# Performance work log

Hardware: AMD Instinct MI355X
Metric: run time of the kernel (lower is better)

## Reference

```python
import jax, jax.numpy as jnp
import numpy as np

D_MODEL = 1024
EXPAND = 2
D_INNER = EXPAND * D_MODEL   # 2048
D_STATE = 16
D_CONV = 4
DT_RANK = 64                  # ceil(d_model / 16)
BATCH = 2
SEQLEN = 1024
DT_MIN, DT_MAX = 0.001, 0.1


def setup_inputs() -> dict:
    key = jax.random.key(0)
    ks = jax.random.split(key, 10)
    s = 0.02
    # dt bias init per Mamba: inv-softplus of dt sampled log-uniform in [dt_min, dt_max]
    u = jax.random.uniform(ks[0], (D_INNER,), jnp.float32)
    dt = jnp.exp(u * (np.log(DT_MAX) - np.log(DT_MIN)) + np.log(DT_MIN))
    dt = jnp.clip(dt, 1e-4, None)
    inv_dt = dt + jnp.log(-jnp.expm1(-dt))
    dt_std = DT_RANK ** -0.5
    A_log = jnp.log(jnp.tile(jnp.arange(1, D_STATE + 1, dtype=jnp.float32), (D_INNER, 1)))
    return {
        "hidden_states": jax.random.normal(ks[1], (BATCH, SEQLEN, D_MODEL), jnp.float32),
        "in_proj_w": jax.random.normal(ks[2], (2 * D_INNER, D_MODEL), jnp.float32) * s,
        "conv1d_w": jax.random.normal(ks[3], (D_INNER, D_CONV), jnp.float32) * s,
        "conv1d_b": jnp.zeros((D_INNER,), jnp.float32),
        "x_proj_w": jax.random.normal(ks[4], (DT_RANK + 2 * D_STATE, D_INNER), jnp.float32) * s,
        "dt_proj_w": jax.random.uniform(ks[5], (D_INNER, DT_RANK), jnp.float32, -dt_std, dt_std),
        "dt_proj_b": inv_dt,
        "A_log": A_log,
        "D_skip": jnp.ones((D_INNER,), jnp.float32),
        "out_proj_w": jax.random.normal(ks[6], (D_MODEL, D_INNER), jnp.float32) * s,
    }


def _mamba_forward(hidden_states, in_proj_w, conv1d_w, conv1d_b, x_proj_w,
                   dt_proj_w, dt_proj_b, A_log, D_skip, out_proj_w):
    B_, L, _ = hidden_states.shape
    # in_proj: (b, l, d_model) -> (b, l, 2*d_inner); split into x and gate z
    xz = jnp.einsum('bld,ed->ble', hidden_states, in_proj_w)
    x, z = xz[..., :D_INNER], xz[..., D_INNER:]
    # causal depthwise conv1d over time (pad left K-1, truncate to L) + SiLU
    xp = jnp.pad(x, ((0, 0), (D_CONV - 1, 0), (0, 0)))
    xc = conv1d_b
    acc = jnp.zeros_like(x)
    for k in range(D_CONV):  # tiny fixed kernel loop
        acc = acc + conv1d_w[:, k] * xp[:, k:k + L, :]
    xc = jax.nn.silu(acc + conv1d_b)
    # input-dependent dt / B / C
    x_dbl = jnp.einsum('bld,rd->blr', xc, x_proj_w)
    dt_lr = x_dbl[..., :DT_RANK]
    Bm = x_dbl[..., DT_RANK:DT_RANK + D_STATE]        # (b, l, n)
    Cm = x_dbl[..., DT_RANK + D_STATE:]               # (b, l, n)
    delta = jax.nn.softplus(jnp.einsum('blr,dr->bld', dt_lr, dt_proj_w) + dt_proj_b)
    A = -jnp.exp(A_log)                               # (d, n)

    def step(state, inputs):
        delta_t, B_t, C_t, u_t = inputs               # (b,d) (b,n) (b,n) (b,d)
        dA = jnp.exp(delta_t[..., None] * A)          # (b, d, n)
        state = state * dA + (delta_t * u_t)[..., None] * B_t[:, None, :]
        y_t = jnp.einsum('bdn,bn->bd', state, C_t)
        return state, y_t

    init = jnp.zeros((B_, D_INNER, D_STATE), delta.dtype)
    scan_in = (jnp.swapaxes(delta, 0, 1), jnp.swapaxes(Bm, 0, 1),
               jnp.swapaxes(Cm, 0, 1), jnp.swapaxes(xc, 0, 1))
    _, ys = jax.lax.scan(step, init, scan_in)         # ys: (l, b, d)
    y = jnp.swapaxes(ys, 0, 1)
    y = y + xc * D_skip                               # skip connection
    y = y * jax.nn.silu(z)                            # gate
    return jnp.einsum('bld,md->blm', y, out_proj_w)   # out_proj (no bias)


def reference(hidden_states, in_proj_w, conv1d_w, conv1d_b, x_proj_w,
              dt_proj_w, dt_proj_b, A_log, D_skip, out_proj_w):
    return _mamba_forward(hidden_states, in_proj_w, conv1d_w, conv1d_b, x_proj_w,
                          dt_proj_w, dt_proj_b, A_log, D_skip, out_proj_w)
```

## Files before the change

kernel.cpp:

```cpp
#include <hip/hip_runtime.h>
#include <hip/hip_bf16.h>
#include <math.h>
#include <stdint.h>

#define D_MODEL 1024
#define D_INNER 2048
#define D_STATE 16
#define D_CONV  4
#define DT_RANK 64
#define BATCH   2
#define SEQLEN  1024
#define M_TOK   (BATCH * SEQLEN)
#define XDBL_W  (DT_RANK + 2 * D_STATE)
#define CHUNKS  64
#define CLEN    (SEQLEN / CHUNKS)
#define KSPLIT  16
#define OSPLIT  4

typedef unsigned short us16;
typedef __bf16 bf16x8 __attribute__((ext_vector_type(8)));
typedef float floatx4 __attribute__((ext_vector_type(4)));

__device__ __forceinline__ float silu_f(float v) {
    return v / (1.0f + __expf(-v));
}
__device__ __forceinline__ float softplus_f(float v) {
    return v > 20.0f ? v : log1pf(__expf(v));
}
__device__ __forceinline__ us16 f2bf(float f) {
    unsigned u = __float_as_uint(f);
    u += 0x7FFF + ((u >> 16) & 1);
    return (us16)(u >> 16);
}
__device__ __forceinline__ float bf2f(us16 h) {
    return __uint_as_float(((unsigned)h) << 16);
}

__device__ __forceinline__ void gload_lds16(const us16* g, us16* l) {
    auto* l3 = reinterpret_cast<__attribute__((address_space(3))) us16*>(
        reinterpret_cast<uintptr_t>(l));
    auto* g1 = reinterpret_cast<const __attribute__((address_space(1))) us16*>(
        reinterpret_cast<uintptr_t>(g));
    __builtin_amdgcn_global_load_lds(g1, l3, 16, 0, 0);
}

__global__ __launch_bounds__(256)
void split_all(const float* __restrict__ hs, const float* __restrict__ iw,
               const float* __restrict__ ow,
               us16* __restrict__ hsh, us16* __restrict__ hsl,
               us16* __restrict__ iwh, us16* __restrict__ iwl,
               us16* __restrict__ owh, us16* __restrict__ owl)
{
    const int b = blockIdx.x;
    const float* src;
    us16 *hi, *lo;
    int rel;
    if (b < 2048)      { src = hs; hi = hsh; lo = hsl; rel = b; }
    else if (b < 6144) { src = iw; hi = iwh; lo = iwl; rel = b - 2048; }
    else               { src = ow; hi = owh; lo = owl; rel = b - 6144; }
    const int i = (rel * 256 + threadIdx.x) * 4;
    const float4 v = *(const float4*)(src + i);
    us16 h0 = f2bf(v.x), h1 = f2bf(v.y), h2 = f2bf(v.z), h3 = f2bf(v.w);
    ushort4 hv = {h0, h1, h2, h3};
    ushort4 lv = {f2bf(v.x - bf2f(h0)), f2bf(v.y - bf2f(h1)),
                  f2bf(v.z - bf2f(h2)), f2bf(v.w - bf2f(h3))};
    *(ushort4*)(hi + i) = hv;
    *(ushort4*)(lo + i) = lv;
}

template<int BN, int MODE>
__global__ __launch_bounds__(256)
void gemm_mfma3(const us16* __restrict__ Ah, const us16* __restrict__ Al,
                const us16* __restrict__ Wh, const us16* __restrict__ Wl,
                int lda, int kLen, float* __restrict__ C0,
                float* __restrict__ C1, int ldc)
{
    constexpr int BM = 128;
    constexpr int NT = BN / 32;
    __shared__ us16 sAh[BM * 32];
    __shared__ us16 sAl[BM * 32];
    __shared__ us16 sWh[BN * 32];
    __shared__ us16 sWl[BN * 32];

    const int tid  = threadIdx.x;
    const int wave = tid >> 6;
    const int lane = tid & 63;
    const int wm   = wave & 1;
    const int wn   = wave >> 1;
    const int m0   = blockIdx.y * BM;
    const int n0   = blockIdx.x * BN;
    const int kBeg = blockIdx.z * kLen;
    const int quad = lane >> 4;
    const int l15  = lane & 15;
    const int sr   = lane >> 2;
    const int spos = lane & 3;

    floatx4 acc[4][NT] = {};

    for (int k0 = 0; k0 < kLen; k0 += 32) {
        __syncthreads();
        {
            int s = wave;
            int row = s * 16 + sr;
            int c = spos ^ ((row >> 1) & 3);
            size_t go = (size_t)(m0 + row) * lda + kBeg + k0 + c * 8;
            gload_lds16(Ah + go, sAh + s * 512);
            gload_lds16(Al + go, sAl + s * 512);
            s = wave + 4;
            row = s * 16 + sr;
            c = spos ^ ((row >> 1) & 3);
            go = (size_t)(m0 + row) * lda + kBeg + k0 + c * 8;
            gload_lds16(Ah + go, sAh + s * 512);
            gload_lds16(Al + go, sAl + s * 512);
        }
        {
            int s = wave;
            int row = s * 16 + sr;
            int c = spos ^ ((row >> 1) & 3);
            size_t go = (size_t)(n0 + row) * lda + kBeg + k0 + c * 8;
            gload_lds16(Wh + go, sWh + s * 512);
            gload_lds16(Wl + go, sWl + s * 512);
            if (BN == 128) {
                s = wave + 4;
                row = s * 16 + sr;
                c = spos ^ ((row >> 1) & 3);
                go = (size_t)(n0 + row) * lda + kBeg + k0 + c * 8;
                gload_lds16(Wh + go, sWh + s * 512);
                gload_lds16(Wl + go, sWl + s * 512);
            }
        }
        __syncthreads();

        bf16x8 ah[4], al[4], bh[NT], bl[NT];
#pragma unroll
        for (int i = 0; i < 4; i++) {
            const int r = wm * 64 + i * 16 + l15;
            const int off = r * 32 + ((quad ^ ((r >> 1) & 3)) * 8);
            ah[i] = *(const bf16x8*)(sAh + off);
            al[i] = *(const bf16x8*)(sAl + off);
        }
#pragma unroll
        for (int j = 0; j < NT; j++) {
            const int r = wn * (BN / 2) + j * 16 + l15;
            const int off = r * 32 + ((quad ^ ((r >> 1) & 3)) * 8);
            bh[j] = *(const bf16x8*)(sWh + off);
            bl[j] = *(const bf16x8*)(sWl + off);
        }
#pragma unroll
        for (int i = 0; i < 4; i++)
#pragma unroll
            for (int j = 0; j < NT; j++) {
                acc[i][j] = __builtin_amdgcn_mfma_f32_16x16x32_bf16(
                    ah[i], bh[j], acc[i][j], 0, 0, 0);
                acc[i][j] = __builtin_amdgcn_mfma_f32_16x16x32_bf16(
                    al[i], bh[j], acc[i][j], 0, 0, 0);
                acc[i][j] = __builtin_amdgcn_mfma_f32_16x16x32_bf16(
                    ah[i], bl[j], acc[i][j], 0, 0, 0);
            }
    }

#pragma unroll
    for (int i = 0; i < 4; i++) {
        const int rowb = m0 + wm * 64 + i * 16 + quad * 4;
#pragma unroll
        for (int j = 0; j < NT; j++) {
            const int col = n0 + wn * (BN / 2) + j * 16 + l15;
#pragma unroll
            for (int r = 0; r < 4; r++) {
                const float v = acc[i][j][r];
                const size_t rr = (size_t)(rowb + r);
                if (MODE == 1) {
                    if (n0 < D_INNER) C0[rr * D_INNER + col] = v;
                    else              C1[rr * D_INNER + (col - D_INNER)] = v;
                } else {
                    C0[((size_t)blockIdx.z * M_TOK + rr) * ldc + col] = v;
                }
            }
        }
    }
}

__global__ __launch_bounds__(256)
void add4_kernel(const float* __restrict__ part, float* __restrict__ out)
{
    const int i = (blockIdx.x * 256 + threadIdx.x) * 4;
    const size_t stride = (size_t)M_TOK * D_MODEL;
    float4 a = *(const float4*)(part + i);
#pragma unroll
    for (int k = 1; k < OSPLIT; k++) {
        const float4 b = *(const float4*)(part + k * stride + i);
        a.x += b.x; a.y += b.y; a.z += b.z; a.w += b.w;
    }
    *(float4*)(out + i) = a;
}

__global__ __launch_bounds__(256)
void gemm_dt(const float* __restrict__ A, int lda,
             const float* __restrict__ W, int ldw,
             float* __restrict__ C0, int ldc,
             const float* __restrict__ bias, int K)
{
    __shared__ float As[16][68];
    __shared__ float Ws[16][68];

    const int tid  = threadIdx.x;
    const int tx   = tid & 15;
    const int ty   = tid >> 4;
    const int n0   = blockIdx.x * 64;
    const int m0   = blockIdx.y * 64;
    const int lrow = tid >> 2;
    const int lkq  = tid & 3;

    float acc[4][4] = {};

    for (int k0 = 0; k0 < K; k0 += 16) {
        const float4 av = *(const float4*)(A + (size_t)(m0 + lrow) * lda + k0 + lkq * 4);
        const float4 wv = *(const float4*)(W + (size_t)(n0 + lrow) * ldw + k0 + lkq * 4);

        __syncthreads();
        As[lkq * 4 + 0][lrow] = av.x;
        As[lkq * 4 + 1][lrow] = av.y;
        As[lkq * 4 + 2][lrow] = av.z;
        As[lkq * 4 + 3][lrow] = av.w;
        Ws[lkq * 4 + 0][lrow] = wv.x;
        Ws[lkq * 4 + 1][lrow] = wv.y;
        Ws[lkq * 4 + 2][lrow] = wv.z;
        Ws[lkq * 4 + 3][lrow] = wv.w;
        __syncthreads();

#pragma unroll
        for (int k = 0; k < 16; k++) {
            const float4 a = *(const float4*)&As[k][ty * 4];
            const float4 w = *(const float4*)&Ws[k][tx * 4];
            const float avv[4] = {a.x, a.y, a.z, a.w};
            const float wvv[4] = {w.x, w.y, w.z, w.w};
#pragma unroll
            for (int i = 0; i < 4; i++)
#pragma unroll
                for (int j = 0; j < 4; j++)
                    acc[i][j] += avv[i] * wvv[j];
        }
    }

    const int mbase = m0 + ty * 4;
    const int nbase = n0 + tx * 4;
#pragma unroll
    for (int i = 0; i < 4; i++)
#pragma unroll
        for (int j = 0; j < 4; j++) {
            const int n = nbase + j;
            C0[(size_t)(mbase + i) * ldc + n] = softplus_f(acc[i][j] + bias[n]);
        }
}

__global__ __launch_bounds__(256)
void gemm_xproj(const float* __restrict__ xg, const float* __restrict__ conv_w,
                const float* __restrict__ conv_b,
                const float* __restrict__ W, float* __restrict__ part)
{
    __shared__ float As[16][68];
    __shared__ float Ws[16][68];

    const int tid  = threadIdx.x;
    const int tx   = tid & 15;
    const int ty   = tid >> 4;
    const int n0   = blockIdx.x * 64;
    const int m0   = blockIdx.y * 64;
    const int kz   = blockIdx.z;
    const int lrow = tid >> 2;
    const int lkq  = tid & 3;

    const float4* cw = (const float4*)conv_w;
    const float4* cb = (const float4*)conv_b;

    float acc[4][4] = {};
    const int kbeg = kz * (D_INNER / KSPLIT);
    const int kend = kbeg + (D_INNER / KSPLIT);

    const int m = m0 + lrow;
    const int t = m & (SEQLEN - 1);

    for (int k0 = kbeg; k0 < kend; k0 += 16) {
        const int dcol = k0 + lkq * 4;
        const float4 w0 = cw[dcol], w1 = cw[dcol + 1], w2 = cw[dcol + 2], w3 = cw[dcol + 3];
        float4 a = cb[dcol >> 2];
        const float* xr = xg + (size_t)m * D_INNER + dcol;
        {
            float4 xk;
            if (t >= 3) { xk = *(const float4*)(xr - 3 * D_INNER);
                a.x += w0.x * xk.x; a.y += w1.x * xk.y; a.z += w2.x * xk.z; a.w += w3.x * xk.w; }
            if (t >= 2) { xk = *(const float4*)(xr - 2 * D_INNER);
                a.x += w0.y * xk.x; a.y += w1.y * xk.y; a.z += w2.y * xk.z; a.w += w3.y * xk.w; }
            if (t >= 1) { xk = *(const float4*)(xr - 1 * D_INNER);
                a.x += w0.z * xk.x; a.y += w1.z * xk.y; a.z += w2.z * xk.z; a.w += w3.z * xk.w; }
            xk = *(const float4*)(xr);
            a.x += w0.w * xk.x; a.y += w1.w * xk.y; a.z += w2.w * xk.z; a.w += w3.w * xk.w;
        }
        const float4 av = make_float4(silu_f(a.x), silu_f(a.y), silu_f(a.z), silu_f(a.w));

        const int wn = n0 + lrow;
        float4 wv = make_float4(0.f, 0.f, 0.f, 0.f);
        if (wn < XDBL_W)
            wv = *(const float4*)(W + (size_t)wn * D_INNER + k0 + lkq * 4);

        __syncthreads();
        As[lkq * 4 + 0][lrow] = av.x;
        As[lkq * 4 + 1][lrow] = av.y;
        As[lkq * 4 + 2][lrow] = av.z;
        As[lkq * 4 + 3][lrow] = av.w;
        Ws[lkq * 4 + 0][lrow] = wv.x;
        Ws[lkq * 4 + 1][lrow] = wv.y;
        Ws[lkq * 4 + 2][lrow] = wv.z;
        Ws[lkq * 4 + 3][lrow] = wv.w;
        __syncthreads();

#pragma unroll
        for (int k = 0; k < 16; k++) {
            const float4 a4 = *(const float4*)&As[k][ty * 4];
            const float4 w4 = *(const float4*)&Ws[k][tx * 4];
            const float avv[4] = {a4.x, a4.y, a4.z, a4.w};
            const float wvv[4] = {w4.x, w4.y, w4.z, w4.w};
#pragma unroll
            for (int i = 0; i < 4; i++)
#pragma unroll
                for (int j = 0; j < 4; j++)
                    acc[i][j] += avv[i] * wvv[j];
        }
    }

    const int mbase = m0 + ty * 4;
    const int nbase = n0 + tx * 4;
#pragma unroll
    for (int i = 0; i < 4; i++)
#pragma unroll
        for (int j = 0; j < 4; j++) {
            const int n = nbase + j;
            if (n < XDBL_W)
                part[((size_t)kz * M_TOK + mbase + i) * XDBL_W + n] = acc[i][j];
        }
}

__global__ __launch_bounds__(256)
void xproj_reduce(const float* __restrict__ part, float* __restrict__ xdbl)
{
    const int i = blockIdx.x * 256 + threadIdx.x;
    float s = 0.f;
#pragma unroll
    for (int k = 0; k < KSPLIT; k++)
        s += part[(size_t)k * M_TOK * XDBL_W + i];
    xdbl[i] = s;
}

__global__ __launch_bounds__(256)
void scan_part(const float* __restrict__ delta, const float* __restrict__ xdbl,
               const float* __restrict__ xg, const float* __restrict__ conv_w,
               const float* __restrict__ conv_b, const float* __restrict__ A_log,
               float* __restrict__ P, float* __restrict__ S)
{
    const int g = blockIdx.x * 256 + threadIdx.x;
    const int d = g & (D_INNER - 1);
    const int c = (g >> 11) & (CHUNKS - 1);
    const int b = g >> 17;

    float An[D_STATE];
#pragma unroll
    for (int n = 0; n < D_STATE; n++)
        An[n] = -__expf(A_log[d * D_STATE + n]);

    const float4 wd = ((const float4*)conv_w)[d];
    const float cb = conv_b[d];

    float p[D_STATE], s[D_STATE];
#pragma unroll
    for (int n = 0; n < D_STATE; n++) { p[n] = 1.f; s[n] = 0.f; }

    const size_t row0 = (size_t)b * SEQLEN + c * CLEN;
    const float* xp = xg + row0 * D_INNER + d;
    float xm3 = 0.f, xm2 = 0.f, xm1 = 0.f;
    if (c > 0) {
        xm3 = xp[-3 * D_INNER];
        xm2 = xp[-2 * D_INNER];
        xm1 = xp[-1 * D_INNER];
    }

#pragma unroll 4
    for (int t = 0; t < CLEN; t++) {
        const size_t row = row0 + t;
        const float xm0 = xp[(size_t)t * D_INNER];
        const float u   = silu_f(cb + wd.x * xm3 + wd.y * xm2 + wd.z * xm1 + wd.w * xm0);
        xm3 = xm2; xm2 = xm1; xm1 = xm0;
        const float dlt  = delta[row * D_INNER + d];
        const float dltu = dlt * u;
        const float4* Bp = (const float4*)(xdbl + row * XDBL_W + DT_RANK);
        const float4 B0 = Bp[0], B1 = Bp[1], B2 = Bp[2], B3 = Bp[3];
        const float Bv[D_STATE] = {B0.x, B0.y, B0.z, B0.w, B1.x, B1.y, B1.z, B1.w,
                                   B2.x, B2.y, B2.z, B2.w, B3.x, B3.y, B3.z, B3.w};
#pragma unroll
        for (int n = 0; n < D_STATE; n++) {
            const float a = __expf(dlt * An[n]);
            s[n] = s[n] * a + dltu * Bv[n];
            p[n] *= a;
        }
    }

    const size_t base = ((size_t)(b * CHUNKS + c) * D_STATE) * D_INNER + d;
#pragma unroll
    for (int n = 0; n < D_STATE; n++) {
        P[base + (size_t)n * D_INNER] = p[n];
        S[base + (size_t)n * D_INNER] = s[n];
    }
}

__global__ __launch_bounds__(256)
void scan_prefix(float* PH, const float* __restrict__ S)
{
    const int g = blockIdx.x * 256 + threadIdx.x;
    const int d = g & (D_INNER - 1);
    const int n = (g >> 11) & (D_STATE - 1);
    const int b = g >> 15;

    float h = 0.f;
    for (int c = 0; c < CHUNKS; c++) {
        const size_t idx = ((size_t)(b * CHUNKS + c) * D_STATE + n) * D_INNER + d;
        const float p = PH[idx];
        const float s = S[idx];
        PH[idx] = h;
        h = s + p * h;
    }
}

__global__ __launch_bounds__(256)
void scan_apply(const float* __restrict__ delta, const float* __restrict__ xdbl,
                const float* __restrict__ xg, const float* __restrict__ conv_w,
                const float* __restrict__ conv_b, const float* __restrict__ A_log,
                const float* __restrict__ D_skip,
                const float* __restrict__ H,
                const float* __restrict__ z,
                us16* __restrict__ yh, us16* __restrict__ yl)
{
    const int g = blockIdx.x * 256 + threadIdx.x;
    const int d = g & (D_INNER - 1);
    const int c = (g >> 11) & (CHUNKS - 1);
    const int b = g >> 17;

    float An[D_STATE];
#pragma unroll
    for (int n = 0; n < D_STATE; n++)
        An[n] = -__expf(A_log[d * D_STATE + n]);

    const float4 wd = ((const float4*)conv_w)[d];
    const float cb = conv_b[d];

    float st[D_STATE];
    const size_t hbase = ((size_t)(b * CHUNKS + c) * D_STATE) * D_INNER + d;
#pragma unroll
    for (int n = 0; n < D_STATE; n++)
        st[n] = H[hbase + (size_t)n * D_INNER];

    const float Dv = D_skip[d];
    const size_t row0 = (size_t)b * SEQLEN + c * CLEN;
    const float* xp = xg + row0 * D_INNER + d;
    float xm3 = 0.f, xm2 = 0.f, xm1 = 0.f;
    if (c > 0) {
        xm3 = xp[-3 * D_INNER];
        xm2 = xp[-2 * D_INNER];
        xm1 = xp[-1 * D_INNER];
    }

#pragma unroll 4
    for (int t = 0; t < CLEN; t++) {
        const size_t row = row0 + t;
        const float xm0 = xp[(size_t)t * D_INNER];
        const float u   = silu_f(cb + wd.x * xm3 + wd.y * xm2 + wd.z * xm1 + wd.w * xm0);
        xm3 = xm2; xm2 = xm1; xm1 = xm0;
        const float dlt  = delta[row * D_INNER + d];
        const float dltu = dlt * u;
        const float4* Bp = (const float4*)(xdbl + row * XDBL_W + DT_RANK);
        const float4 B0 = Bp[0], B1 = Bp[1], B2 = Bp[2], B3 = Bp[3];
        const float4* Cp = (const float4*)(xdbl + row * XDBL_W + DT_RANK + D_STATE);
        const float4 C0 = Cp[0], C1 = Cp[1], C2 = Cp[2], C3 = Cp[3];
        const float Bv[D_STATE] = {B0.x, B0.y, B0.z, B0.w, B1.x, B1.y, B1.z, B1.w,
                                   B2.x, B2.y, B2.z, B2.w, B3.x, B3.y, B3.z, B3.w};
        const float Cv[D_STATE] = {C0.x, C0.y, C0.z, C0.w, C1.x, C1.y, C1.z, C1.w,
                                   C2.x, C2.y, C2.z, C2.w, C3.x, C3.y, C3.z, C3.w};
        float y = 0.f;
#pragma unroll
        for (int n = 0; n < D_STATE; n++) {
            const float a = __expf(dlt * An[n]);
            st[n] = st[n] * a + dltu * Bv[n];
            y += st[n] * Cv[n];
        }
        const float yv = (y + u * Dv) * silu_f(z[row * D_INNER + d]);
        const us16 h = f2bf(yv);
        yh[row * D_INNER + d] = h;
        yl[row * D_INNER + d] = f2bf(yv - bf2f(h));
    }
}

extern "C" void kernel_launch(void* const* d_in, const int* in_sizes, int n_in,
                              void* d_out, int out_size, void* d_ws, size_t ws_size,
                              hipStream_t stream)
{
    const float* hs         = (const float*)d_in[0];
    const float* in_proj_w  = (const float*)d_in[1];
    const float* conv_w     = (const float*)d_in[2];
    const float* conv_b     = (const float*)d_in[3];
    const float* x_proj_w   = (const float*)d_in[4];
    const float* dt_proj_w  = (const float*)d_in[5];
    const float* dt_proj_b  = (const float*)d_in[6];
    const float* A_log      = (const float*)d_in[7];
    const float* D_skip     = (const float*)d_in[8];
    const float* out_proj_w = (const float*)d_in[9];
    float* out = (float*)d_out;

    char* base = (char*)d_ws;
    const size_t MB = 1u << 20;
    float* xbuf  = (float*)(base);
    float* zbuf  = (float*)(base + 16 * MB);
    float* opart = (float*)(base);
    float* dbuf  = (float*)(base + 32 * MB);
    float* xdbl  = (float*)(base + 48 * MB);
    us16*  iwh   = (us16*)(base + 49 * MB);
    us16*  iwl   = (us16*)(base + 57 * MB);
    float* part  = (float*)(base + 49 * MB);
    float* Pbuf  = (float*)(base + 49 * MB);
    us16*  hsh   = (us16*)(base + 65 * MB);
    us16*  hsl   = (us16*)(base + 69 * MB);
    float* Sbuf  = (float*)(base + 65 * MB);
    us16*  ybh   = (us16*)(base + 65 * MB);
    us16*  ybl   = (us16*)(base + 73 * MB);
    us16*  owh   = (us16*)(base + 81 * MB);
    us16*  owl   = (us16*)(base + 85 * MB);

    const dim3 blk(256);

    split_all<<<8192, blk, 0, stream>>>(hs, in_proj_w, out_proj_w,
                                        hsh, hsl, iwh, iwl, owh, owl);

    gemm_mfma3<128, 1><<<dim3((2 * D_INNER) / 128, M_TOK / 128), blk, 0, stream>>>(
        hsh, hsl, iwh, iwl, D_MODEL, D_MODEL, xbuf, zbuf, D_INNER);

    gemm_xproj<<<dim3(2, M_TOK / 64, KSPLIT), blk, 0, stream>>>(
        xbuf, conv_w, conv_b, x_proj_w, part);
    xproj_reduce<<<(M_TOK * XDBL_W) / 256, blk, 0, stream>>>(part, xdbl);

    gemm_dt<<<dim3(D_INNER / 64, M_TOK / 64), blk, 0, stream>>>(
        xdbl, XDBL_W, dt_proj_w, DT_RANK, dbuf, D_INNER, dt_proj_b, DT_RANK);

    scan_part<<<(BATCH * CHUNKS * D_INNER) / 256, blk, 0, stream>>>(
        dbuf, xdbl, xbuf, conv_w, conv_b, A_log, Pbuf, Sbuf);
    scan_prefix<<<(BATCH * D_STATE * D_INNER) / 256, blk, 0, stream>>>(
        Pbuf, Sbuf);
    scan_apply<<<(BATCH * CHUNKS * D_INNER) / 256, blk, 0, stream>>>(
        dbuf, xdbl, xbuf, conv_w, conv_b, A_log, D_skip, Pbuf, zbuf, ybh, ybl);

    gemm_mfma3<128, 2><<<dim3(D_MODEL / 128, M_TOK / 128, OSPLIT), blk, 0, stream>>>(
        ybh, ybl, owh, owl, D_INNER, D_INNER / OSPLIT, opart, nullptr, D_MODEL);
    add4_kernel<<<(M_TOK * D_MODEL) / 1024, blk, 0, stream>>>(opart, out);
}
```

Baseline: 324.0 us.

## Cover all 96 x_proj columns per block and retile in_proj GEMM

The x_proj GEMM now has each block compute all 96 output columns (4x6 per thread) instead of two 64-wide column tiles. The old layout padded the second tile with zeros and recomputed the causal conv and SiLU of the activations once per tile. KSPLIT is doubled to keep enough blocks in flight, which doubles the partial-sum traffic the reduce kernel must read. The in_proj GEMM also switches to a 64-wide N tile, giving twice as many blocks.

```diff
diff --git a/kernel.cpp b/kernel.cpp
--- a/kernel.cpp
+++ b/kernel.cpp
@@ -14,7 +14,7 @@
 #define XDBL_W  (DT_RANK + 2 * D_STATE)
 #define CHUNKS  64
 #define CLEN    (SEQLEN / CHUNKS)
-#define KSPLIT  16
+#define KSPLIT  32
 #define OSPLIT  4
 
 typedef unsigned short us16;
@@ -259,21 +259,20 @@
                 const float* __restrict__ W, float* __restrict__ part)
 {
     __shared__ float As[16][68];
-    __shared__ float Ws[16][68];
+    __shared__ float Ws[16][100];
 
     const int tid  = threadIdx.x;
     const int tx   = tid & 15;
     const int ty   = tid >> 4;
-    const int n0   = blockIdx.x * 64;
-    const int m0   = blockIdx.y * 64;
-    const int kz   = blockIdx.z;
+    const int m0   = blockIdx.x * 64;
+    const int kz   = blockIdx.y;
     const int lrow = tid >> 2;
     const int lkq  = tid & 3;
 
     const float4* cw = (const float4*)conv_w;
     const float4* cb = (const float4*)conv_b;
 
-    float acc[4][4] = {};
+    float acc[4][6] = {};
     const int kbeg = kz * (D_INNER / KSPLIT);
     const int kend = kbeg + (D_INNER / KSPLIT);
 
@@ -298,10 +297,10 @@
         }
         const float4 av = make_float4(silu_f(a.x), silu_f(a.y), silu_f(a.z), silu_f(a.w));
 
-        const int wn = n0 + lrow;
-        float4 wv = make_float4(0.f, 0.f, 0.f, 0.f);
-        if (wn < XDBL_W)
-            wv = *(const float4*)(W + (size_t)wn * D_INNER + k0 + lkq * 4);
+        const float4 wv = *(const float4*)(W + (size_t)lrow * D_INNER + k0 + lkq * 4);
+        float4 wv2 = make_float4(0.f, 0.f, 0.f, 0.f);
+        if (tid < 128)
+            wv2 = *(const float4*)(W + (size_t)(64 + lrow) * D_INNER + k0 + lkq * 4);
 
         __syncthreads();
         As[lkq * 4 + 0][lrow] = av.x;
@@ -312,32 +311,36 @@
         Ws[lkq * 4 + 1][lrow] = wv.y;
         Ws[lkq * 4 + 2][lrow] = wv.z;
         Ws[lkq * 4 + 3][lrow] = wv.w;
+        if (tid < 128) {
+            Ws[lkq * 4 + 0][64 + lrow] = wv2.x;
+            Ws[lkq * 4 + 1][64 + lrow] = wv2.y;
+            Ws[lkq * 4 + 2][64 + lrow] = wv2.z;
+            Ws[lkq * 4 + 3][64 + lrow] = wv2.w;
+        }
         __syncthreads();
 
 #pragma unroll
         for (int k = 0; k < 16; k++) {
             const float4 a4 = *(const float4*)&As[k][ty * 4];
-            const float4 w4 = *(const float4*)&Ws[k][tx * 4];
             const float avv[4] = {a4.x, a4.y, a4.z, a4.w};
-            const float wvv[4] = {w4.x, w4.y, w4.z, w4.w};
+            float wvv[6];
+#pragma unroll
+            for (int j = 0; j < 6; j++) wvv[j] = Ws[k][tx * 6 + j];
 #pragma unroll
             for (int i = 0; i < 4; i++)
 #pragma unroll
-                for (int j = 0; j < 4; j++)
+                for (int j = 0; j < 6; j++)
                     acc[i][j] += avv[i] * wvv[j];
         }
     }
 
     const int mbase = m0 + ty * 4;
-    const int nbase = n0 + tx * 4;
+    const int nbase = tx * 6;
 #pragma unroll
     for (int i = 0; i < 4; i++)
 #pragma unroll
-        for (int j = 0; j < 4; j++) {
-            const int n = nbase + j;
-            if (n < XDBL_W)
-                part[((size_t)kz * M_TOK + mbase + i) * XDBL_W + n] = acc[i][j];
-        }
+        for (int j = 0; j < 6; j++)
+            part[((size_t)kz * M_TOK + mbase + i) * XDBL_W + nbase + j] = acc[i][j];
 }
 
 __global__ __launch_bounds__(256)
@@ -345,7 +348,7 @@
 {
     const int i = blockIdx.x * 256 + threadIdx.x;
     float s = 0.f;
-#pragma unroll
+#pragma unroll 8
     for (int k = 0; k < KSPLIT; k++)
         s += part[(size_t)k * M_TOK * XDBL_W + i];
     xdbl[i] = s;
@@ -537,10 +540,10 @@
     split_all<<<8192, blk, 0, stream>>>(hs, in_proj_w, out_proj_w,
                                         hsh, hsl, iwh, iwl, owh, owl);
 
-    gemm_mfma3<128, 1><<<dim3((2 * D_INNER) / 128, M_TOK / 128), blk, 0, stream>>>(
+    gemm_mfma3<64, 1><<<dim3((2 * D_INNER) / 64, M_TOK / 128), blk, 0, stream>>>(
         hsh, hsl, iwh, iwl, D_MODEL, D_MODEL, xbuf, zbuf, D_INNER);
 
-    gemm_xproj<<<dim3(2, M_TOK / 64, KSPLIT), blk, 0, stream>>>(
+    gemm_xproj<<<dim3(M_TOK / 64, KSPLIT), blk, 0, stream>>>(
         xbuf, conv_w, conv_b, x_proj_w, part);
     xproj_reduce<<<(M_TOK * XDBL_W) / 256, blk, 0, stream>>>(part, xdbl);
 
```

After: 323.6 us. No clear change (-0.1%).
